# Performance work log

Hardware: AMD Instinct MI355X
Metric: run time of the kernel (lower is better)

The kernel has to match this reference:

```python
import jax, jax.numpy as jnp
import numpy as np

B, T, V, F, O, K_ORDER = 16, 16, 512, 64, 64, 3


def setup_inputs() -> dict:
    key = jax.random.key(0)
    k1, k2, k3, k4 = jax.random.split(key, 4)
    x = jax.random.normal(k1, (B, T, V, F), dtype=jnp.float32)
    Att = jax.random.uniform(k2, (B, V, V), dtype=jnp.float32)
    S = jax.random.uniform(k3, (B, T, V, V), dtype=jnp.float32)
    Theta = jax.random.uniform(k4, (K_ORDER, F, O), dtype=jnp.float32) * 0.1
    return {"x": x, "Att": Att, "S": S, "Theta": Theta}


def reference(x, Att, S, Theta):
    # x: (B,T,V,F); Att: (B,V,V); S: (B,T,V,V); Theta: (k,F,O)
    Bv, Tv, Vv, Fv = x.shape
    k_order = Theta.shape[0]
    # symmetrize via elementwise min with transpose over the two vertex dims
    S = jnp.minimum(S, jnp.swapaxes(S, -1, -2))
    # per-timestep: D = diag(sum(A, axis=1)) (sum over rows, i.e. axis=2 here)
    deg = S.sum(axis=2)                      # (B,T,V)
    eye = jnp.eye(Vv, dtype=x.dtype)
    # L_t = D - A - I
    L_t = deg[..., None] * eye - S - eye     # (B,T,V,V)
    Att_b = Att[:, None]                     # (B,1,V,V) broadcast over T

    # Chebyshev recurrence is ELEMENTWISE in the original code: T_k = 2*L_t*T_{k-1} - T_{k-2}
    Tkm2 = jnp.broadcast_to(eye, L_t.shape)  # T_0 = I
    Tkm1 = L_t                               # T_1 = L_t
    # rhs = (T_k * Att)^T @ x  ->  sum_u (T_k*Att)[u,v] * x[u,f]; then @ Theta[k]
    out = jnp.einsum('btuv,btuf,fo->btvo', Tkm2 * Att_b, x, Theta[0])
    if k_order > 1:
        out = out + jnp.einsum('btuv,btuf,fo->btvo', Tkm1 * Att_b, x, Theta[1])
    for i in range(2, k_order):
        Tk = 2.0 * L_t * Tkm1 - Tkm2
        out = out + jnp.einsum('btuv,btuf,fo->btvo', Tk * Att_b, x, Theta[i])
        Tkm2, Tkm1 = Tkm1, Tk
    return jax.nn.relu(out)                  # (B,T,V,O)
```

## Files before the change

kernel.cpp:

```cpp
#include <hip/hip_runtime.h>

#define VV 512
#define FF 64
#define OO 64
#define YELEMS 8388608

#define C1_OFF    0u
#define C2_OFF    67108864u
#define Y1F8_OFF  134217728u
#define Y2F8_OFF  142606336u
#define YB_OFF    150994944u
#define DEGP_OFF  201326592u
#define SDG_OFF   205520896u
#define ADG_OFF   206045184u
#define WS_NEED   206569472u

using f32x4 = __attribute__((ext_vector_type(4))) float;
using s16x8 = __attribute__((ext_vector_type(8))) short;
using u16x4 = __attribute__((ext_vector_type(4))) unsigned short;

__device__ __forceinline__ short f2bf(float f) {
    union { float f; unsigned int u; } v; v.f = f;
    unsigned int u = v.u;
    u += 0x7fffu + ((u >> 16) & 1u);
    return (short)(u >> 16);
}
__device__ __forceinline__ float bf2f(unsigned short u) {
    union { unsigned int u; float f; } v; v.u = ((unsigned int)u) << 16; return v.f;
}
__device__ __forceinline__ int swz(int row) { return (row >> 1) & 7; }

__device__ __forceinline__ void gload16(const void* g, void* l) {
    __builtin_amdgcn_global_load_lds(
        (const __attribute__((address_space(1))) unsigned int*)g,
        (__attribute__((address_space(3))) unsigned int*)l, 16, 0, 0);
}

__device__ __forceinline__ void coef_pass(
    const float (*Tuv)[65], const float (*Tvu)[65], const float (*Auv)[65],
    float (*degred)[64], unsigned char* c1out, unsigned char* c2out,
    int tid, bool isdiag, float* SdgW, float* AdgW)
{
    const int uq = (tid & 15) * 4;
    const int vrow = tid >> 4;
    float dd0 = 0.f, dd1 = 0.f, dd2 = 0.f, dd3 = 0.f;
    #pragma unroll
    for (int it = 0; it < 4; ++it) {
        const int v = vrow + it * 16;
        float c1v[4], c2v[4];
        #pragma unroll
        for (int e = 0; e < 4; ++e) {
            float sm = fminf(Tuv[uq + e][v], Tvu[v][uq + e]);
            float a  = Auv[uq + e][v];
            if (e == 0) dd0 += sm; else if (e == 1) dd1 += sm;
            else if (e == 2) dd2 += sm; else dd3 += sm;
            float c1 = -a * sm;
            float c2 = (a + a) * (sm * sm);
            if (isdiag && (uq + e == v)) {
                c1 = 0.f; c2 = 0.f;
                SdgW[v] = sm; AdgW[v] = a;
            }
            c1v[e] = c1; c2v[e] = c2;
        }
        int w1 = __builtin_amdgcn_cvt_pk_fp8_f32(c1v[0], c1v[1], 0, false);
        w1     = __builtin_amdgcn_cvt_pk_fp8_f32(c1v[2], c1v[3], w1, true);
        int w2 = __builtin_amdgcn_cvt_pk_fp8_f32(c2v[0], c2v[1], 0, false);
        w2     = __builtin_amdgcn_cvt_pk_fp8_f32(c2v[2], c2v[3], w2, true);
        *(int*)(c1out + (size_t)v * VV + uq) = w1;
        *(int*)(c2out + (size_t)v * VV + uq) = w2;
    }
    degred[vrow][uq + 0] = dd0;
    degred[vrow][uq + 1] = dd1;
    degred[vrow][uq + 2] = dd2;
    degred[vrow][uq + 3] = dd3;
}

__global__ __launch_bounds__(256, 2)
void coef_kernel(const float* __restrict__ S, const float* __restrict__ Att,
                 unsigned char* __restrict__ ws)
{
    __shared__ float Tij[64][65];
    __shared__ float Tji[64][65];
    __shared__ float Aij[64][65];
    __shared__ float Aji[64][65];
    __shared__ float degA[16][64];
    __shared__ float degB[16][64];

    const int tid = threadIdx.x;
    const int bt = blockIdx.x / 36;
    int p = blockIdx.x - bt * 36;
    int i = 0;
    while (p >= 8 - i) { p -= 8 - i; ++i; }
    const int j = i + p;
    const int b = bt >> 4;
    const int u0i = i * 64, u0j = j * 64;

    const float* Sbt = S + (size_t)bt * VV * VV;
    const float* Abt = Att + (size_t)b * VV * VV;

    {
        const int r = tid >> 2, c4 = (tid & 3) * 16;
        const float* gij = Sbt + (size_t)(u0i + r) * VV + u0j + c4;
        const float* gji = Sbt + (size_t)(u0j + r) * VV + u0i + c4;
        const float* aij = Abt + (size_t)(u0i + r) * VV + u0j + c4;
        const float* aji = Abt + (size_t)(u0j + r) * VV + u0i + c4;
        #pragma unroll
        for (int w = 0; w < 4; ++w) {
            float4 t = ((const float4*)gij)[w];
            Tij[r][c4 + w * 4 + 0] = t.x; Tij[r][c4 + w * 4 + 1] = t.y;
            Tij[r][c4 + w * 4 + 2] = t.z; Tij[r][c4 + w * 4 + 3] = t.w;
        }
        #pragma unroll
        for (int w = 0; w < 4; ++w) {
            float4 t = ((const float4*)gji)[w];
            Tji[r][c4 + w * 4 + 0] = t.x; Tji[r][c4 + w * 4 + 1] = t.y;
            Tji[r][c4 + w * 4 + 2] = t.z; Tji[r][c4 + w * 4 + 3] = t.w;
        }
        #pragma unroll
        for (int w = 0; w < 4; ++w) {
            float4 t = ((const float4*)aij)[w];
            Aij[r][c4 + w * 4 + 0] = t.x; Aij[r][c4 + w * 4 + 1] = t.y;
            Aij[r][c4 + w * 4 + 2] = t.z; Aij[r][c4 + w * 4 + 3] = t.w;
        }
        #pragma unroll
        for (int w = 0; w < 4; ++w) {
            float4 t = ((const float4*)aji)[w];
            Aji[r][c4 + w * 4 + 0] = t.x; Aji[r][c4 + w * 4 + 1] = t.y;
            Aji[r][c4 + w * 4 + 2] = t.z; Aji[r][c4 + w * 4 + 3] = t.w;
        }
    }
    __syncthreads();

    unsigned char* c1w = ws + C1_OFF + (size_t)bt * (VV * VV);
    unsigned char* c2w = ws + C2_OFF + (size_t)bt * (VV * VV);
    float* SdgW = (float*)(ws + SDG_OFF) + (size_t)bt * VV;
    float* AdgW = (float*)(ws + ADG_OFF) + (size_t)bt * VV;
    float* degpW = (float*)(ws + DEGP_OFF) + (size_t)bt * 8 * VV;

    coef_pass(Tij, Tji, Aij, degA,
              c1w + (size_t)u0j * VV + u0i, c2w + (size_t)u0j * VV + u0i,
              tid, (i == j), SdgW + u0j, AdgW + u0j);
    if (i < j) {
        coef_pass(Tji, Tij, Aji, degB,
                  c1w + (size_t)u0i * VV + u0j, c2w + (size_t)u0i * VV + u0j,
                  tid, false, SdgW, AdgW);
    }
    __syncthreads();

    if (tid < 64) {
        float s = 0.f;
        #pragma unroll
        for (int k = 0; k < 16; ++k) s += degA[k][tid];
        degpW[(size_t)j * VV + u0i + tid] = s;
    } else if (tid < 128 && i < j) {
        float s = 0.f;
        #pragma unroll
        for (int k = 0; k < 16; ++k) s += degB[k][tid - 64];
        degpW[(size_t)i * VV + u0j + (tid - 64)] = s;
    }
}

__global__ __launch_bounds__(256, 4)
void y_kernel2(const float* __restrict__ x, const float* __restrict__ Theta,
               unsigned char* __restrict__ ws)
{
    __shared__ __align__(16) unsigned char smem[32768];
    short* xT = (short*)(smem);

    const int tid = threadIdx.x, lane = tid & 63, q = tid >> 6;
    const int g = lane >> 4, nbase = lane & 15;
    const int bt = blockIdx.x >> 3;
    const int u0 = (blockIdx.x & 7) * 64;

    {
        const float* xp = x + ((size_t)(bt * VV + u0 + lane)) * FF + q * 16;
        float4 a0 = ((const float4*)xp)[0];
        float4 a1 = ((const float4*)xp)[1];
        float4 a2 = ((const float4*)xp)[2];
        float4 a3 = ((const float4*)xp)[3];
        float v[16] = {a0.x,a0.y,a0.z,a0.w, a1.x,a1.y,a1.z,a1.w,
                       a2.x,a2.y,a2.z,a2.w, a3.x,a3.y,a3.z,a3.w};
        s16x8 p0, p1;
        #pragma unroll
        for (int e = 0; e < 8; ++e) { p0[e] = f2bf(v[e]); p1[e] = f2bf(v[8 + e]); }
        const int fs = swz(lane);
        *(s16x8*)&xT[lane * 64 + (((q * 2)     ^ fs) * 8)] = p0;
        *(s16x8*)&xT[lane * 64 + (((q * 2 + 1) ^ fs) * 8)] = p1;
    }
    #pragma unroll
    for (int k = 0; k < 3; ++k) {
        short* tk = (short*)(smem + 8192 + k * 8192);
        s16x8 p0, p1;
        #pragma unroll
        for (int e = 0; e < 8; ++e) {
            p0[e] = f2bf(Theta[k * FF * OO + (q * 16 + e) * OO + lane]);
            p1[e] = f2bf(Theta[k * FF * OO + (q * 16 + 8 + e) * OO + lane]);
        }
        const int fs = swz(lane);
        *(s16x8*)&tk[lane * 64 + (((q * 2)     ^ fs) * 8)] = p0;
        *(s16x8*)&tk[lane * 64 + (((q * 2 + 1) ^ fs) * 8)] = p1;
    }
    __syncthreads();

    f32x4 zero = {0.f, 0.f, 0.f, 0.f};
    f32x4 acc[3][4];
    #pragma unroll
    for (int k = 0; k < 3; ++k)
        #pragma unroll
        for (int nt = 0; nt < 4; ++nt) acc[k][nt] = zero;

    const int mrow = q * 16 + nbase;
    const int moff = mrow * 64, ms = swz(mrow);
    #pragma unroll
    for (int kk = 0; kk < 2; ++kk) {
        const int slotA = kk * 4 + g;
        s16x8 a = *(const s16x8*)&xT[moff + ((slotA ^ ms) * 8)];
        #pragma unroll
        for (int nt = 0; nt < 4; ++nt) {
            const int nrow = nt * 16 + nbase;
            const int nad = nrow * 64 + ((slotA ^ swz(nrow)) * 8);
            #pragma unroll
            for (int k = 0; k < 3; ++k) {
                s16x8 bb = *(const s16x8*)&((short*)(smem + 8192 + k * 8192))[nad];
                acc[k][nt] = __builtin_amdgcn_mfma_f32_16x16x32_bf16(a, bb, acc[k][nt], 0, 0, 0);
            }
        }
    }
    unsigned short* yb = (unsigned short*)(ws + YB_OFF);
    unsigned char* y1f8 = ws + Y1F8_OFF + (size_t)bt * 32768;
    unsigned char* y2f8 = ws + Y2F8_OFF + (size_t)bt * 32768;
    #pragma unroll
    for (int k = 0; k < 3; ++k) {
        #pragma unroll
        for (int nt = 0; nt < 4; ++nt) {
            const int o = nt * 16 + nbase;
            const int u = u0 + q * 16 + g * 4;
            u16x4 pk;
            #pragma unroll
            for (int r = 0; r < 4; ++r) pk[r] = (unsigned short)f2bf(acc[k][nt][r]);
            *(u16x4*)&yb[(size_t)k * YELEMS + ((size_t)(bt * 64 + o)) * VV + u] = pk;
            if (k >= 1) {
                const int s = u >> 3;
                const int sw = (s & ~7) | ((s & 7) ^ (o & 7));
                const int ad = o * 512 + sw * 8 + (u & 4);
                int w = __builtin_amdgcn_cvt_pk_fp8_f32(acc[k][nt][0], acc[k][nt][1], 0, false);
                w     = __builtin_amdgcn_cvt_pk_fp8_f32(acc[k][nt][2], acc[k][nt][3], w, true);
                if (k == 1) *(int*)(y1f8 + ad) = w;
                else        *(int*)(y2f8 + ad) = w;
            }
        }
    }
}

__global__ __launch_bounds__(256, 2)
void cheb_b(const unsigned char* __restrict__ ws, float* __restrict__ out)
{
    __shared__ __align__(16) unsigned char yLds[65536];

    const int tid = threadIdx.x, lane = tid & 63, q = tid >> 6;
    const int g = lane >> 4, nbase = lane & 15;

    const int wg = blockIdx.x;
    const int bt = (wg & 7) + ((wg >> 6) << 3);
    const int vt = (wg >> 3) & 7;
    const int v0 = vt * 64;

    const int mrow = q * 16 + nbase;
    const int vg   = v0 + mrow;

    {
        const unsigned char* y1img = ws + Y1F8_OFF + (size_t)bt * 32768;
        const unsigned char* y2img = ws + Y2F8_OFF + (size_t)bt * 32768;
        const int wo = q * 1024 + lane * 16;
        #pragma unroll
        for (int i = 0; i < 8; ++i) {
            gload16(y1img + i * 4096 + wo, (char*)yLds + i * 4096 + q * 1024);
            gload16(y2img + i * 4096 + wo, (char*)yLds + 32768 + i * 4096 + q * 1024);
        }
    }

    const unsigned char* c1r = ws + C1_OFF + (size_t)bt * (VV * VV) + (size_t)vg * VV + g * 8;
    const unsigned char* c2r = ws + C2_OFF + (size_t)bt * (VV * VV) + (size_t)vg * VV + g * 8;
    long c1f[16], c2f[16];
    #pragma unroll
    for (int it = 0; it < 16; ++it) {
        c1f[it] = *(const long*)(c1r + it * 32);
        c2f[it] = *(const long*)(c2r + it * 32);
    }

    __syncthreads();

    f32x4 zero = {0.f, 0.f, 0.f, 0.f};
    f32x4 acc[4];
    #pragma unroll
    for (int i = 0; i < 4; ++i) acc[i] = zero;

    #pragma unroll
    for (int ut = 0; ut < 8; ++ut) {
        #pragma unroll
        for (int kk = 0; kk < 2; ++kk) {
            const int it = ut * 2 + kk;
            const long a1 = c1f[it];
            const long a2 = c2f[it];
            #pragma unroll
            for (int nt = 0; nt < 4; ++nt) {
                const int o = nt * 16 + nbase;
                const int ad = o * 512 + (ut * 8 + ((kk * 4 + g) ^ (o & 7))) * 8;
                long b1 = *(const long*)&yLds[ad];
                long b2 = *(const long*)&yLds[32768 + ad];
                acc[nt] = __builtin_amdgcn_mfma_f32_16x16x32_fp8_fp8(a1, b1, acc[nt], 0, 0, 0);
                acc[nt] = __builtin_amdgcn_mfma_f32_16x16x32_fp8_fp8(a2, b2, acc[nt], 0, 0, 0);
            }
        }
    }

    const unsigned short* y0g = (const unsigned short*)(ws + YB_OFF) + (size_t)bt * 64 * VV;
    const unsigned short* y1g = y0g + (size_t)YELEMS;
    const unsigned short* y2g = y0g + (size_t)2 * YELEMS;
    const float* degp = (const float*)(ws + DEGP_OFF) + (size_t)bt * 8 * VV;
    const float* SdgW = (const float*)(ws + SDG_OFF) + (size_t)bt * VV;
    const float* AdgW = (const float*)(ws + ADG_OFF) + (size_t)bt * VV;

    float* obt = out + (size_t)bt * VV * OO;
    #pragma unroll
    for (int r = 0; r < 4; ++r) {
        const int vloc = q * 16 + g * 4 + r;
        const int vgr = v0 + vloc;
        float dv = 0.f;
        #pragma unroll
        for (int s = 0; s < 8; ++s) dv += degp[(size_t)s * VV + vgr];
        const float Ad = AdgW[vgr];
        const float Sd = SdgW[vgr];
        const float Ld = dv - Sd - 1.0f;
        const float w1 = Ad * Ld;
        const float w2 = Ad * (2.0f * Ld * Ld - 1.0f);
        #pragma unroll
        for (int nt = 0; nt < 4; ++nt) {
            const int oo = nt * 16 + nbase;
            const size_t yi = (size_t)oo * VV + vgr;
            float y0v = bf2f(y0g[yi]);
            float y1v = bf2f(y1g[yi]);
            float y2v = bf2f(y2g[yi]);
            float val = acc[nt][r] + Ad * y0v + w1 * y1v + w2 * y2v;
            obt[(size_t)vgr * OO + oo] = fmaxf(val, 0.0f);
        }
    }
}

__global__ __launch_bounds__(256, 4)
void y_kernel_fb(const float* __restrict__ x, const float* __restrict__ Theta,
                 unsigned short* __restrict__ yT)
{
    __shared__ __align__(16) unsigned char smem[32768];
    short* xT = (short*)(smem);
    const int tid = threadIdx.x, lane = tid & 63, q = tid >> 6;
    const int g = lane >> 4, nbase = lane & 15;
    const int bt = blockIdx.x >> 3;
    const int u0 = (blockIdx.x & 7) * 64;
    {
        const float* xp = x + ((size_t)(bt * VV + u0 + lane)) * FF + q * 16;
        float4 a0 = ((const float4*)xp)[0];
        float4 a1 = ((const float4*)xp)[1];
        float4 a2 = ((const float4*)xp)[2];
        float4 a3 = ((const float4*)xp)[3];
        float v[16] = {a0.x,a0.y,a0.z,a0.w, a1.x,a1.y,a1.z,a1.w,
                       a2.x,a2.y,a2.z,a2.w, a3.x,a3.y,a3.z,a3.w};
        s16x8 p0, p1;
        #pragma unroll
        for (int e = 0; e < 8; ++e) { p0[e] = f2bf(v[e]); p1[e] = f2bf(v[8 + e]); }
        const int fs = swz(lane);
        *(s16x8*)&xT[lane * 64 + (((q * 2)     ^ fs) * 8)] = p0;
        *(s16x8*)&xT[lane * 64 + (((q * 2 + 1) ^ fs) * 8)] = p1;
    }
    #pragma unroll
    for (int k = 0; k < 3; ++k) {
        short* tk = (short*)(smem + 8192 + k * 8192);
        s16x8 p0, p1;
        #pragma unroll
        for (int e = 0; e < 8; ++e) {
            p0[e] = f2bf(Theta[k * FF * OO + (q * 16 + e) * OO + lane]);
            p1[e] = f2bf(Theta[k * FF * OO + (q * 16 + 8 + e) * OO + lane]);
        }
        const int fs = swz(lane);
        *(s16x8*)&tk[lane * 64 + (((q * 2)     ^ fs) * 8)] = p0;
        *(s16x8*)&tk[lane * 64 + (((q * 2 + 1) ^ fs) * 8)] = p1;
    }
    __syncthreads();
    f32x4 zero = {0.f, 0.f, 0.f, 0.f};
    f32x4 acc[3][4];
    #pragma unroll
    for (int k = 0; k < 3; ++k)
        #pragma unroll
        for (int nt = 0; nt < 4; ++nt) acc[k][nt] = zero;
    const int mrow = q * 16 + nbase;
    const int moff = mrow * 64, ms = swz(mrow);
    #pragma unroll
    for (int kk = 0; kk < 2; ++kk) {
        const int slotA = kk * 4 + g;
        s16x8 a = *(const s16x8*)&xT[moff + ((slotA ^ ms) * 8)];
        #pragma unroll
        for (int nt = 0; nt < 4; ++nt) {
            const int nrow = nt * 16 + nbase;
            const int nad = nrow * 64 + ((slotA ^ swz(nrow)) * 8);
            #pragma unroll
            for (int k = 0; k < 3; ++k) {
                s16x8 bb = *(const s16x8*)&((short*)(smem + 8192 + k * 8192))[nad];
                acc[k][nt] = __builtin_amdgcn_mfma_f32_16x16x32_bf16(a, bb, acc[k][nt], 0, 0, 0);
            }
        }
    }
    #pragma unroll
    for (int k = 0; k < 3; ++k) {
        #pragma unroll
        for (int nt = 0; nt < 4; ++nt) {
            const int o = nt * 16 + nbase;
            const int u = u0 + q * 16 + g * 4;
            u16x4 pk;
            #pragma unroll
            for (int r = 0; r < 4; ++r) pk[r] = (unsigned short)f2bf(acc[k][nt][r]);
            *(u16x4*)&yT[(size_t)k * YELEMS + ((size_t)(bt * 64 + o)) * VV + u] = pk;
        }
    }
}

__global__ __launch_bounds__(256, 4)
void cheb_main_fb(const float* __restrict__ S, const float* __restrict__ Att,
                  const unsigned short* __restrict__ yT, float* __restrict__ out)
{
    const int tid = threadIdx.x, lane = tid & 63, q = tid >> 6;
    const int g = lane >> 4, nbase = lane & 15;
    const int wg = blockIdx.x;
    const int bt = (wg & 7) + ((wg >> 6) << 3);
    const int vt = (wg >> 3) & 7;
    const int v0 = vt * 64;
    const int b  = bt >> 4;
    const float* Sbt = S + (size_t)bt * VV * VV;
    const float* Abt = Att + (size_t)b * VV * VV;
    const unsigned short* y0g = yT + (size_t)bt * 64 * VV;
    const unsigned short* y1g = y0g + (size_t)YELEMS;
    const unsigned short* y2g = y0g + (size_t)2 * YELEMS;
    const int mrow = q * 16 + nbase;
    const int vg   = v0 + mrow;
    const float* Srow = Sbt + (size_t)vg * VV;
    const float* Scol = Sbt + vg;
    const float* Acol = Abt + vg;
    f32x4 zero = {0.f, 0.f, 0.f, 0.f};
    f32x4 acc[4];
    #pragma unroll
    for (int i = 0; i < 4; ++i) acc[i] = zero;
    float da0 = 0.f, da1 = 0.f, adg = 0.f, sdg = 0.f;
    #pragma unroll
    for (int ut = 0; ut < 8; ++ut) {
        const int u0t = ut * 64;
        #pragma unroll
        for (int kk = 0; kk < 2; ++kk) {
            const int ub = u0t + (kk * 4 + g) * 8;
            s16x8 b10 = *(const s16x8*)&y1g[(size_t)(0 * 16 + nbase) * VV + ub];
            s16x8 b11 = *(const s16x8*)&y1g[(size_t)(1 * 16 + nbase) * VV + ub];
            s16x8 b12 = *(const s16x8*)&y1g[(size_t)(2 * 16 + nbase) * VV + ub];
            s16x8 b13 = *(const s16x8*)&y1g[(size_t)(3 * 16 + nbase) * VV + ub];
            f32x4 r0 = *(const f32x4*)(Srow + ub);
            f32x4 r1 = *(const f32x4*)(Srow + ub + 4);
            s16x8 a1, a2;
            #pragma unroll
            for (int e = 0; e < 8; ++e) {
                float sc = Scol[(size_t)(ub + e) * VV];
                float av = Acol[(size_t)(ub + e) * VV];
                float rv = (e < 4) ? r0[e] : r1[e - 4];
                float sm = fminf(sc, rv);
                if (e & 1) da1 += sm; else da0 += sm;
                float c1 = -av * sm;
                float c2 = (av + av) * (sm * sm);
                if (ub + e == vg) { c1 = 0.f; c2 = 0.f; adg = av; sdg = sm; }
                a1[e] = f2bf(c1);
                a2[e] = f2bf(c2);
            }
            acc[0] = __builtin_amdgcn_mfma_f32_16x16x32_bf16(a1, b10, acc[0], 0, 0, 0);
            acc[1] = __builtin_amdgcn_mfma_f32_16x16x32_bf16(a1, b11, acc[1], 0, 0, 0);
            acc[2] = __builtin_amdgcn_mfma_f32_16x16x32_bf16(a1, b12, acc[2], 0, 0, 0);
            acc[3] = __builtin_amdgcn_mfma_f32_16x16x32_bf16(a1, b13, acc[3], 0, 0, 0);
            s16x8 b20 = *(const s16x8*)&y2g[(size_t)(0 * 16 + nbase) * VV + ub];
            s16x8 b21 = *(const s16x8*)&y2g[(size_t)(1 * 16 + nbase) * VV + ub];
            s16x8 b22 = *(const s16x8*)&y2g[(size_t)(2 * 16 + nbase) * VV + ub];
            s16x8 b23 = *(const s16x8*)&y2g[(size_t)(3 * 16 + nbase) * VV + ub];
            acc[0] = __builtin_amdgcn_mfma_f32_16x16x32_bf16(a2, b20, acc[0], 0, 0, 0);
            acc[1] = __builtin_amdgcn_mfma_f32_16x16x32_bf16(a2, b21, acc[1], 0, 0, 0);
            acc[2] = __builtin_amdgcn_mfma_f32_16x16x32_bf16(a2, b22, acc[2], 0, 0, 0);
            acc[3] = __builtin_amdgcn_mfma_f32_16x16x32_bf16(a2, b23, acc[3], 0, 0, 0);
        }
    }
    float da = da0 + da1;
    da  += __shfl_xor(da, 16);  da  += __shfl_xor(da, 32);
    adg += __shfl_xor(adg, 16); adg += __shfl_xor(adg, 32);
    sdg += __shfl_xor(sdg, 16); sdg += __shfl_xor(sdg, 32);
    float* obt = out + (size_t)bt * VV * OO;
    #pragma unroll
    for (int r = 0; r < 4; ++r) {
        const int vloc = q * 16 + g * 4 + r;
        const int src  = g * 4 + r;
        const float Ad = __shfl(adg, src);
        const float dv = __shfl(da,  src);
        const float Sd = __shfl(sdg, src);
        const float Ld = dv - Sd - 1.0f;
        const float w1 = Ad * Ld;
        const float w2 = Ad * (2.0f * Ld * Ld - 1.0f);
        const int vgr = v0 + vloc;
        #pragma unroll
        for (int nt = 0; nt < 4; ++nt) {
            const int oo = nt * 16 + nbase;
            const size_t yi = (size_t)oo * VV + vgr;
            float y0v = bf2f(y0g[yi]);
            float y1v = bf2f(y1g[yi]);
            float y2v = bf2f(y2g[yi]);
            float val = acc[nt][r] + Ad * y0v + w1 * y1v + w2 * y2v;
            obt[(size_t)vgr * OO + oo] = fmaxf(val, 0.0f);
        }
    }
}

extern "C" void kernel_launch(void* const* d_in, const int* in_sizes, int n_in,
                              void* d_out, int out_size, void* d_ws, size_t ws_size,
                              hipStream_t stream) {
    (void)in_sizes; (void)n_in; (void)out_size;
    const float* x   = (const float*)d_in[0];
    const float* Att = (const float*)d_in[1];
    const float* S   = (const float*)d_in[2];
    const float* Th  = (const float*)d_in[3];
    float* outp = (float*)d_out;
    if (ws_size >= (size_t)WS_NEED) {
        unsigned char* ws = (unsigned char*)d_ws;
        hipLaunchKernelGGL(coef_kernel, dim3(9216), dim3(256), 0, stream, S, Att, ws);
        hipLaunchKernelGGL(y_kernel2, dim3(2048), dim3(256), 0, stream, x, Th, ws);
        hipLaunchKernelGGL(cheb_b, dim3(2048), dim3(256), 0, stream, ws, outp);
    } else {
        unsigned short* yT = (unsigned short*)d_ws;
        hipLaunchKernelGGL(y_kernel_fb, dim3(2048), dim3(256), 0, stream, x, Th, yT);
        hipLaunchKernelGGL(cheb_main_fb, dim3(2048), dim3(256), 0, stream, S, Att, yT, outp);
    }
}
```

Measured before the change: 200.6 us.

## Switch cheb_b to 32x32x16 fp8 MFMA with repacked coefficient and y layouts

The main fp8 GEMM in cheb_b now uses 32x32x16 MFMA tiles instead of 16x16x32. Each wave covers a 32x32 output tile and loads 16-byte coefficient vectors, so coef_kernel writes the coefficients in an interleaved column order to match. The bf16 y tensors are stored in v-major (u,o) layout so the epilogue reads them coalesced, and the fp8 y LDS images use a 16-way swizzle. Per-vertex degree and diagonal terms are staged once in LDS instead of each thread re-reading them from global memory. The cost is scattered 2-byte stores in the y producer and extra barriers in cheb_b.

```diff
diff --git a/kernel.cpp b/kernel.cpp
--- a/kernel.cpp
+++ b/kernel.cpp
@@ -9,15 +9,17 @@
 #define C2_OFF    67108864u
 #define Y1F8_OFF  134217728u
 #define Y2F8_OFF  142606336u
-#define YB_OFF    150994944u
+#define YVO_OFF   150994944u
 #define DEGP_OFF  201326592u
 #define SDG_OFF   205520896u
 #define ADG_OFF   206045184u
 #define WS_NEED   206569472u
 
-using f32x4 = __attribute__((ext_vector_type(4))) float;
-using s16x8 = __attribute__((ext_vector_type(8))) short;
-using u16x4 = __attribute__((ext_vector_type(4))) unsigned short;
+using f32x4  = __attribute__((ext_vector_type(4))) float;
+using f32x16 = __attribute__((ext_vector_type(16))) float;
+using s16x8  = __attribute__((ext_vector_type(8))) short;
+using u16x4  = __attribute__((ext_vector_type(4))) unsigned short;
+using i64x2  = __attribute__((ext_vector_type(2))) long;
 
 __device__ __forceinline__ short f2bf(float f) {
     union { float f; unsigned int u; } v; v.f = f;
@@ -38,11 +40,14 @@
 
 __device__ __forceinline__ void coef_pass(
     const float (*Tuv)[65], const float (*Tvu)[65], const float (*Auv)[65],
-    float (*degred)[64], unsigned char* c1out, unsigned char* c2out,
+    float (*degred)[64], unsigned char* c1row0, unsigned char* c2row0, int u0c,
     int tid, bool isdiag, float* SdgW, float* AdgW)
 {
     const int uq = (tid & 15) * 4;
     const int vrow = tid >> 4;
+    const int ug = u0c + uq;
+    const int s  = ug >> 3;
+    const int du = (s & 1) * 256 + (s >> 1) * 8 + (uq & 4);
     float dd0 = 0.f, dd1 = 0.f, dd2 = 0.f, dd3 = 0.f;
     #pragma unroll
     for (int it = 0; it < 4; ++it) {
@@ -66,8 +71,8 @@
         w1     = __builtin_amdgcn_cvt_pk_fp8_f32(c1v[2], c1v[3], w1, true);
         int w2 = __builtin_amdgcn_cvt_pk_fp8_f32(c2v[0], c2v[1], 0, false);
         w2     = __builtin_amdgcn_cvt_pk_fp8_f32(c2v[2], c2v[3], w2, true);
-        *(int*)(c1out + (size_t)v * VV + uq) = w1;
-        *(int*)(c2out + (size_t)v * VV + uq) = w2;
+        *(int*)(c1row0 + (size_t)v * VV + du) = w1;
+        *(int*)(c2row0 + (size_t)v * VV + du) = w2;
     }
     degred[vrow][uq + 0] = dd0;
     degred[vrow][uq + 1] = dd1;
@@ -138,11 +143,11 @@
     float* degpW = (float*)(ws + DEGP_OFF) + (size_t)bt * 8 * VV;
 
     coef_pass(Tij, Tji, Aij, degA,
-              c1w + (size_t)u0j * VV + u0i, c2w + (size_t)u0j * VV + u0i,
+              c1w + (size_t)u0j * VV, c2w + (size_t)u0j * VV, u0i,
               tid, (i == j), SdgW + u0j, AdgW + u0j);
     if (i < j) {
         coef_pass(Tji, Tij, Aji, degB,
-                  c1w + (size_t)u0i * VV + u0j, c2w + (size_t)u0i * VV + u0j,
+                  c1w + (size_t)u0i * VV, c2w + (size_t)u0i * VV, u0j,
                   tid, false, SdgW, AdgW);
     }
     __syncthreads();
@@ -226,7 +231,7 @@
             }
         }
     }
-    unsigned short* yb = (unsigned short*)(ws + YB_OFF);
+    unsigned short* yvo = (unsigned short*)(ws + YVO_OFF);
     unsigned char* y1f8 = ws + Y1F8_OFF + (size_t)bt * 32768;
     unsigned char* y2f8 = ws + Y2F8_OFF + (size_t)bt * 32768;
     #pragma unroll
@@ -235,13 +240,13 @@
         for (int nt = 0; nt < 4; ++nt) {
             const int o = nt * 16 + nbase;
             const int u = u0 + q * 16 + g * 4;
-            u16x4 pk;
             #pragma unroll
-            for (int r = 0; r < 4; ++r) pk[r] = (unsigned short)f2bf(acc[k][nt][r]);
-            *(u16x4*)&yb[(size_t)k * YELEMS + ((size_t)(bt * 64 + o)) * VV + u] = pk;
+            for (int r = 0; r < 4; ++r)
+                yvo[(size_t)k * YELEMS + (size_t)bt * 32768 + (size_t)(u + r) * OO + o] =
+                    (unsigned short)f2bf(acc[k][nt][r]);
             if (k >= 1) {
                 const int s = u >> 3;
-                const int sw = (s & ~7) | ((s & 7) ^ (o & 7));
+                const int sw = (s & ~15) | ((s & 15) ^ (o & 15));
                 const int ad = o * 512 + sw * 8 + (u & 4);
                 int w = __builtin_amdgcn_cvt_pk_fp8_f32(acc[k][nt][0], acc[k][nt][1], 0, false);
                 w     = __builtin_amdgcn_cvt_pk_fp8_f32(acc[k][nt][2], acc[k][nt][3], w, true);
@@ -257,93 +262,99 @@
 {
     __shared__ __align__(16) unsigned char yLds[65536];
 
-    const int tid = threadIdx.x, lane = tid & 63, q = tid >> 6;
-    const int g = lane >> 4, nbase = lane & 15;
+    const int tid = threadIdx.x, lane = tid & 63;
+    const int wv = tid >> 6;
+    const int vh = wv >> 1, oh = wv & 1;
+    const int rl = lane & 31, hi = lane >> 5;
 
     const int wg = blockIdx.x;
     const int bt = (wg & 7) + ((wg >> 6) << 3);
     const int vt = (wg >> 3) & 7;
     const int v0 = vt * 64;
 
-    const int mrow = q * 16 + nbase;
-    const int vg   = v0 + mrow;
-
     {
         const unsigned char* y1img = ws + Y1F8_OFF + (size_t)bt * 32768;
         const unsigned char* y2img = ws + Y2F8_OFF + (size_t)bt * 32768;
-        const int wo = q * 1024 + lane * 16;
+        const int wo = wv * 1024 + lane * 16;
         #pragma unroll
         for (int i = 0; i < 8; ++i) {
-            gload16(y1img + i * 4096 + wo, (char*)yLds + i * 4096 + q * 1024);
-            gload16(y2img + i * 4096 + wo, (char*)yLds + 32768 + i * 4096 + q * 1024);
-        }
-    }
-
-    const unsigned char* c1r = ws + C1_OFF + (size_t)bt * (VV * VV) + (size_t)vg * VV + g * 8;
-    const unsigned char* c2r = ws + C2_OFF + (size_t)bt * (VV * VV) + (size_t)vg * VV + g * 8;
-    long c1f[16], c2f[16];
-    #pragma unroll
-    for (int it = 0; it < 16; ++it) {
-        c1f[it] = *(const long*)(c1r + it * 32);
-        c2f[it] = *(const long*)(c2r + it * 32);
-    }
-
-    __syncthreads();
-
-    f32x4 zero = {0.f, 0.f, 0.f, 0.f};
-    f32x4 acc[4];
-    #pragma unroll
-    for (int i = 0; i < 4; ++i) acc[i] = zero;
-
-    #pragma unroll
-    for (int ut = 0; ut < 8; ++ut) {
-        #pragma unroll
-        for (int kk = 0; kk < 2; ++kk) {
-            const int it = ut * 2 + kk;
-            const long a1 = c1f[it];
-            const long a2 = c2f[it];
+            gload16(y1img + i * 4096 + wo, (char*)yLds + i * 4096 + wv * 1024);
+            gload16(y2img + i * 4096 + wo, (char*)yLds + 32768 + i * 4096 + wv * 1024);
+        }
+    }
+
+    const size_t crow = (size_t)(v0 + vh * 32 + rl) * VV + hi * 256;
+    const unsigned char* c1base = ws + C1_OFF + (size_t)bt * (VV * VV) + crow;
+    const unsigned char* c2base = ws + C2_OFF + (size_t)bt * (VV * VV) + crow;
+    i64x2 c1p[16], c2p[16];
+    #pragma unroll
+    for (int jj = 0; jj < 16; ++jj) {
+        c1p[jj] = *(const i64x2*)(c1base + jj * 16);
+        c2p[jj] = *(const i64x2*)(c2base + jj * 16);
+    }
+
+    __syncthreads();
+
+    f32x16 acc;
+    #pragma unroll
+    for (int i = 0; i < 16; ++i) acc[i] = 0.f;
+
+    const int yrow = (oh * 32 + rl) * 512;
+    const int x15  = rl & 15;
+
+    #pragma unroll
+    for (int it = 0; it < 32; ++it) {
+        const long a1 = c1p[it >> 1][it & 1];
+        const long a2 = c2p[it >> 1][it & 1];
+        const int s  = it * 2 + hi;
+        const int sw = (s & ~15) | ((s & 15) ^ x15);
+        const int ad = yrow + sw * 8;
+        const long b1 = *(const long*)&yLds[ad];
+        const long b2 = *(const long*)&yLds[32768 + ad];
+        acc = __builtin_amdgcn_mfma_f32_32x32x16_fp8_fp8(a1, b1, acc, 0, 0, 0);
+        acc = __builtin_amdgcn_mfma_f32_32x32x16_fp8_fp8(a2, b2, acc, 0, 0, 0);
+    }
+
+    __syncthreads();
+    {
+        float* ep = (float*)yLds;
+        const float* degp = (const float*)(ws + DEGP_OFF) + (size_t)bt * 8 * VV;
+        const float* SdgW = (const float*)(ws + SDG_OFF) + (size_t)bt * VV;
+        const float* AdgW = (const float*)(ws + ADG_OFF) + (size_t)bt * VV;
+        if (tid < 64) {
+            float dv = 0.f;
             #pragma unroll
-            for (int nt = 0; nt < 4; ++nt) {
-                const int o = nt * 16 + nbase;
-                const int ad = o * 512 + (ut * 8 + ((kk * 4 + g) ^ (o & 7))) * 8;
-                long b1 = *(const long*)&yLds[ad];
-                long b2 = *(const long*)&yLds[32768 + ad];
-                acc[nt] = __builtin_amdgcn_mfma_f32_16x16x32_fp8_fp8(a1, b1, acc[nt], 0, 0, 0);
-                acc[nt] = __builtin_amdgcn_mfma_f32_16x16x32_fp8_fp8(a2, b2, acc[nt], 0, 0, 0);
-            }
-        }
-    }
-
-    const unsigned short* y0g = (const unsigned short*)(ws + YB_OFF) + (size_t)bt * 64 * VV;
-    const unsigned short* y1g = y0g + (size_t)YELEMS;
-    const unsigned short* y2g = y0g + (size_t)2 * YELEMS;
-    const float* degp = (const float*)(ws + DEGP_OFF) + (size_t)bt * 8 * VV;
-    const float* SdgW = (const float*)(ws + SDG_OFF) + (size_t)bt * VV;
-    const float* AdgW = (const float*)(ws + ADG_OFF) + (size_t)bt * VV;
-
+            for (int s = 0; s < 8; ++s) dv += degp[(size_t)s * VV + v0 + tid];
+            ep[tid] = dv;
+        } else if (tid < 128) {
+            ep[64 + (tid - 64)] = SdgW[v0 + (tid - 64)];
+        } else if (tid < 192) {
+            ep[128 + (tid - 128)] = AdgW[v0 + (tid - 128)];
+        }
+    }
+    __syncthreads();
+
+    const float* ep = (const float*)yLds;
+    const unsigned short* yvo = (const unsigned short*)(ws + YVO_OFF) + (size_t)bt * 32768;
     float* obt = out + (size_t)bt * VV * OO;
-    #pragma unroll
-    for (int r = 0; r < 4; ++r) {
-        const int vloc = q * 16 + g * 4 + r;
+    const int o = oh * 32 + rl;
+
+    #pragma unroll
+    for (int r = 0; r < 16; ++r) {
+        const int vloc = vh * 32 + (r & 3) + 8 * (r >> 2) + 4 * hi;
         const int vgr = v0 + vloc;
-        float dv = 0.f;
-        #pragma unroll
-        for (int s = 0; s < 8; ++s) dv += degp[(size_t)s * VV + vgr];
-        const float Ad = AdgW[vgr];
-        const float Sd = SdgW[vgr];
+        const float dv = ep[vloc];
+        const float Sd = ep[64 + vloc];
+        const float Ad = ep[128 + vloc];
         const float Ld = dv - Sd - 1.0f;
         const float w1 = Ad * Ld;
         const float w2 = Ad * (2.0f * Ld * Ld - 1.0f);
-        #pragma unroll
-        for (int nt = 0; nt < 4; ++nt) {
-            const int oo = nt * 16 + nbase;
-            const size_t yi = (size_t)oo * VV + vgr;
-            float y0v = bf2f(y0g[yi]);
-            float y1v = bf2f(y1g[yi]);
-            float y2v = bf2f(y2g[yi]);
-            float val = acc[nt][r] + Ad * y0v + w1 * y1v + w2 * y2v;
-            obt[(size_t)vgr * OO + oo] = fmaxf(val, 0.0f);
-        }
+        const size_t yi = (size_t)vgr * OO + o;
+        float y0v = bf2f(yvo[yi]);
+        float y1v = bf2f(yvo[(size_t)YELEMS + yi]);
+        float y2v = bf2f(yvo[(size_t)2 * YELEMS + yi]);
+        float val = acc[r] + Ad * y0v + w1 * y1v + w2 * y2v;
+        obt[(size_t)vgr * OO + o] = fmaxf(val, 0.0f);
     }
 }
 
```

Result: slower. 219.2 us (+9.3%).
